# Performance work log

Hardware: AMD Instinct MI355X
Metric: run time of the kernel (lower is better)

Reference implementation:

```python
import jax, jax.numpy as jnp
import numpy as np

EMBED_DIM = 512
NUM_HEADS = 8
HEAD_DIM = EMBED_DIM // NUM_HEADS
SEQ = 1024
BSZ = 8
T1 = 0.6
T2 = 0.4
MAX_NEG = -jnp.finfo(jnp.float32).max


def setup_inputs() -> dict:
    key = jax.random.key(0)
    ks = jax.random.split(key, 10)
    shp = (SEQ, BSZ, EMBED_DIM)
    inv = 1.0 / np.sqrt(EMBED_DIM)
    return {
        "query": jax.random.normal(ks[0], shp, jnp.float32),
        "key": jax.random.normal(ks[1], shp, jnp.float32),
        "value": jax.random.normal(ks[2], shp, jnp.float32),
        "query_sem": jax.random.normal(ks[3], shp, jnp.float32),
        "key_sem": jax.random.normal(ks[4], shp, jnp.float32),
        "sem_map": jax.random.uniform(ks[5], (SEQ, SEQ), jnp.float32),
        "in_proj_weight": jax.random.normal(ks[6], (3 * EMBED_DIM, EMBED_DIM), jnp.float32) * inv,
        "in_proj_bias": jnp.zeros((3 * EMBED_DIM,), jnp.float32),
        "out_proj_weight": jax.random.normal(ks[7], (EMBED_DIM, EMBED_DIM), jnp.float32) * inv,
        "out_proj_bias": jnp.zeros((EMBED_DIM,), jnp.float32),
    }


def _heads(x):
    # [T, B, E] -> [B*H, T, head_dim]
    T, B, E = x.shape
    return jnp.transpose(x.reshape(T, B * NUM_HEADS, HEAD_DIM), (1, 0, 2))


def _attn_path(qx, kx, vx, sem_map, Wi, bi, Wo, bo, ssa):
    # packed in-projection (generic path: q, k, v are distinct tensors)
    Wq, Wk, Wv = jnp.split(Wi, 3, axis=0)
    bq, bk, bv = jnp.split(bi, 3)
    q = _heads(qx @ Wq.T + bq)
    k = _heads(kx @ Wk.T + bk)
    v = _heads(vx @ Wv.T + bv)
    scale = 1.0 / np.sqrt(HEAD_DIM)
    scores = jnp.einsum("bte,bse->bts", q * scale, k)  # [B*H, T, S]
    scores = jnp.where(sem_map[None, :, :] < 0.5, MAX_NEG, scores)
    if ssa:
        # keep only the argmax entry per row, others set to max_neg
        idx = jnp.argmax(scores, axis=-1)  # [B*H, T]
        keep = jnp.arange(scores.shape[-1])[None, None, :] == idx[..., None]
        scores = jnp.where(keep, scores, MAX_NEG)
    w = jax.nn.softmax(scores, axis=-1)
    o = jnp.einsum("bts,bse->bte", w, v)  # [B*H, T, head_dim]
    o = jnp.transpose(o, (1, 0, 2)).reshape(SEQ, BSZ, EMBED_DIM)
    return o @ Wo.T + bo


def reference(query, key, value, query_sem, key_sem, sem_map, in_proj_weight, in_proj_bias, out_proj_weight, out_proj_bias):
    # SCA: semantic q/k attend, style value
    x_sca = _attn_path(query_sem, key_sem, value, sem_map, in_proj_weight, in_proj_bias, out_proj_weight, out_proj_bias, ssa=False)
    # SSA: content/style q/k, hard-argmax sparsified attention
    x_ssa = _attn_path(query, key, value, sem_map, in_proj_weight, in_proj_bias, out_proj_weight, out_proj_bias, ssa=True)
    return T1 * x_sca + T2 * x_ssa
```

## Files before the change

kernel.cpp:

```cpp
#include <hip/hip_runtime.h>
#include <float.h>


namespace {
constexpr int kSeq = 1024;
constexpr int kBsz = 8;
constexpr int kEmb = 512;
constexpr int kHD  = 64;
constexpr float kT1 = 0.6f;
constexpr float kT2 = 0.4f;
constexpr float kScale = 0.125f;
constexpr float kMargin = 0.125f;
constexpr int kCap = 256;
}

typedef short bf16x8 __attribute__((ext_vector_type(8)));
typedef float f32x4  __attribute__((ext_vector_type(4)));

union FragU { uint4 u4; bf16x8 f; uint u[4]; };

__device__ __forceinline__ ushort f2bf(float f) {
  uint u = __float_as_uint(f);
  u += 0x7fff + ((u >> 16) & 1);
  return (ushort)(u >> 16);
}
__device__ __forceinline__ uint pack2(float lo, float hi) {
  return (uint)f2bf(lo) | ((uint)f2bf(hi) << 16);
}
__device__ __forceinline__ float bf2f(uint h) {
  return __uint_as_float(h << 16);
}
__device__ __forceinline__ uint monokey(float v) {
  uint u = __float_as_uint(v);
  return (u & 0x80000000u) ? ~u : (u | 0x80000000u);
}

__global__ void smask_prep(const float* __restrict__ SEM,
                           unsigned long long* __restrict__ SMASK) {
  const int t = blockIdx.x;
  const int w4 = threadIdx.x >> 6;
  const int lane = threadIdx.x & 63;
#pragma unroll
  for (int i = 0; i < 4; ++i) {
    const int word = (w4 << 2) + i;
    const float v = SEM[t * kSeq + (word << 6) + lane];
    unsigned long long m = __ballot(v >= 0.5f);
    if (lane == 0) SMASK[t * 16 + word] = m;
  }
}

__global__ __launch_bounds__(256, 4) void proj_v4(
    const float* __restrict__ Xq, const float* __restrict__ Xk,
    const float* __restrict__ W, const float* __restrict__ bias,
    float* __restrict__ OutQ, float* __restrict__ OutK,
    ushort* __restrict__ ShQ, ushort* __restrict__ ShK)
{
  __shared__ float As[32 * 132];
  __shared__ float Bs[32 * 68];

  const int z = blockIdx.z;
  const float* X = z ? Xk : Xq;
  float* Out = z ? OutK : OutQ;
  ushort* shadow = z ? ShK : ShQ;
  const int woff = z << 9;
  const float sscale = z ? 1.0f : kScale;

  const int mBase = blockIdx.x << 7;
  const int nBase = blockIdx.y << 6;
  const int tid = threadIdx.x;
  const int tx = tid & 15;
  const int my = tid >> 4;
  const int ar = tid >> 1, ah = (tid & 1) << 4;
  const int br = tid >> 2, bk = (tid & 3) << 3;

  float acc[8][4];
#pragma unroll
  for (int i = 0; i < 8; ++i)
#pragma unroll
    for (int j = 0; j < 4; ++j) acc[i][j] = 0.f;

  const float* xp = X + (size_t)(mBase + ar) * kEmb + ah;
  const float* wp = W + (size_t)(woff + nBase + br) * kEmb + bk;

  float4 a0 = ((const float4*)xp)[0];
  float4 a1 = ((const float4*)xp)[1];
  float4 a2 = ((const float4*)xp)[2];
  float4 a3 = ((const float4*)xp)[3];
  float4 b0 = ((const float4*)wp)[0];
  float4 b1 = ((const float4*)wp)[1];

  for (int k0 = 0; k0 < kEmb; k0 += 32) {
    __syncthreads();
    {
      float av[16] = {a0.x, a0.y, a0.z, a0.w, a1.x, a1.y, a1.z, a1.w,
                      a2.x, a2.y, a2.z, a2.w, a3.x, a3.y, a3.z, a3.w};
#pragma unroll
      for (int i = 0; i < 16; ++i) As[(ah + i) * 132 + ar] = av[i];
      float bv[8] = {b0.x, b0.y, b0.z, b0.w, b1.x, b1.y, b1.z, b1.w};
#pragma unroll
      for (int i = 0; i < 8; ++i) Bs[(bk + i) * 68 + br] = bv[i];
    }
    __syncthreads();

    const int kn = k0 + 32;
    if (kn < kEmb) {
      a0 = ((const float4*)(xp + kn))[0];
      a1 = ((const float4*)(xp + kn))[1];
      a2 = ((const float4*)(xp + kn))[2];
      a3 = ((const float4*)(xp + kn))[3];
      b0 = ((const float4*)(wp + kn))[0];
      b1 = ((const float4*)(wp + kn))[1];
    }

#pragma unroll 8
    for (int k = 0; k < 32; ++k) {
      float4 A0 = *(const float4*)&As[k * 132 + (my << 3)];
      float4 A1 = *(const float4*)&As[k * 132 + (my << 3) + 4];
      float4 Bv = *(const float4*)&Bs[k * 68 + (tx << 2)];
      float aa[8] = {A0.x, A0.y, A0.z, A0.w, A1.x, A1.y, A1.z, A1.w};
      float bb[4] = {Bv.x, Bv.y, Bv.z, Bv.w};
#pragma unroll
      for (int i = 0; i < 8; ++i)
#pragma unroll
        for (int j = 0; j < 4; ++j)
          acc[i][j] = fmaf(aa[i], bb[j], acc[i][j]);
    }
  }

#pragma unroll
  for (int i = 0; i < 8; ++i) {
    const int m = mBase + (my << 3) + i;
#pragma unroll
    for (int j = 0; j < 4; ++j) {
      const int n = nBase + (tx << 2) + j;
      const float v = acc[i][j] + bias[woff + n];
      const int oi = (((m & 7) << 3) + (n >> 6)) * (kSeq * kHD) +
                     ((m >> 3) << 6) + (n & 63);
      Out[oi] = v;
      shadow[oi] = f2bf(v * sscale);
    }
  }
}

__global__ __launch_bounds__(256, 2) void gemm_bf16(
    const float* __restrict__ X0, const float* __restrict__ X1,
    const float* __restrict__ X2, const ushort* __restrict__ X16,
    const float* __restrict__ W, const float* __restrict__ bias,
    float* __restrict__ OutF, ushort* __restrict__ Out16,
    int woffBase, int aMode, int outMode, float scale0)
{
  __shared__ uint As[128 * 20];
  __shared__ uint Bs[64 * 20];

  const int z = blockIdx.z;
  const float* X = (z == 0) ? X0 : (z == 1) ? X1 : X2;
  const int woff = woffBase + (z << 9);
  const float scale = (z == 0) ? scale0 : 1.0f;
  const size_t zoff = (size_t)z * ((size_t)kSeq * kBsz * kEmb);

  const int mBase = blockIdx.x << 7;
  const int nBase = blockIdx.y << 6;
  const int tid = threadIdx.x;
  const int w = tid >> 6;
  const int l = tid & 63;
  const int l15 = l & 15;
  const int quad = l >> 4;
  const int wm = w & 1, wn = w >> 1;

  const int srow = tid >> 1;
  const int shalf = tid & 1;

  f32x4 acc[4][2];
#pragma unroll
  for (int mi = 0; mi < 4; ++mi)
#pragma unroll
    for (int ni = 0; ni < 2; ++ni) acc[mi][ni] = (f32x4){0.f, 0.f, 0.f, 0.f};

  uint4 qa0, qa1;
  float4 ra0, ra1, ra2, ra3;
  float4 rb0, rb1, rb2, rb3;

#define GLOAD(kk) do {                                                     \
    if (aMode == 2) {                                                      \
      const uint* src_ = (const uint*)X16 + (size_t)(mBase + srow) * 256 + \
                         ((kk) >> 1) + (shalf << 3);                       \
      qa0 = ((const uint4*)src_)[0];                                       \
      qa1 = ((const uint4*)src_)[1];                                       \
    } else {                                                               \
      const float* xp_ = X + (size_t)(mBase + srow) * kEmb + (kk) +        \
                         (shalf << 4);                                     \
      ra0 = ((const float4*)xp_)[0];                                       \
      ra1 = ((const float4*)xp_)[1];                                       \
      ra2 = ((const float4*)xp_)[2];                                       \
      ra3 = ((const float4*)xp_)[3];                                       \
    }                                                                      \
    if (tid < 128) {                                                       \
      const float* wp_ = W + (size_t)(woff + nBase + srow) * kEmb + (kk) + \
                         (shalf << 4);                                     \
      rb0 = ((const float4*)wp_)[0];                                       \
      rb1 = ((const float4*)wp_)[1];                                       \
      rb2 = ((const float4*)wp_)[2];                                       \
      rb3 = ((const float4*)wp_)[3];                                       \
    }                                                                      \
  } while (0)

  GLOAD(0);

  for (int k0 = 0; k0 < kEmb; k0 += 32) {
    uint4 ah0, ah1, bw0, bw1;
    if (aMode == 2) {
      ah0 = qa0; ah1 = qa1;
    } else {
      ah0 = make_uint4(pack2(ra0.x, ra0.y), pack2(ra0.z, ra0.w),
                       pack2(ra1.x, ra1.y), pack2(ra1.z, ra1.w));
      ah1 = make_uint4(pack2(ra2.x, ra2.y), pack2(ra2.z, ra2.w),
                       pack2(ra3.x, ra3.y), pack2(ra3.z, ra3.w));
    }
    if (tid < 128) {
      bw0 = make_uint4(pack2(rb0.x, rb0.y), pack2(rb0.z, rb0.w),
                       pack2(rb1.x, rb1.y), pack2(rb1.z, rb1.w));
      bw1 = make_uint4(pack2(rb2.x, rb2.y), pack2(rb2.z, rb2.w),
                       pack2(rb3.x, rb3.y), pack2(rb3.z, rb3.w));
    }
    __syncthreads();
    {
      uint* dst = As + srow * 20 + (shalf << 3);
      ((uint4*)dst)[0] = ah0;
      ((uint4*)dst)[1] = ah1;
      if (tid < 128) {
        uint* db = Bs + srow * 20 + (shalf << 3);
        ((uint4*)db)[0] = bw0;
        ((uint4*)db)[1] = bw1;
      }
    }
    __syncthreads();

    if (k0 + 32 < kEmb) GLOAD(k0 + 32);

    FragU aF[4], bF[2];
#pragma unroll
    for (int ni = 0; ni < 2; ++ni)
      bF[ni].u4 = *(const uint4*)(Bs + ((wn << 5) + (ni << 4) + l15) * 20 + (quad << 2));
#pragma unroll
    for (int mi = 0; mi < 4; ++mi)
      aF[mi].u4 = *(const uint4*)(As + ((wm << 6) + (mi << 4) + l15) * 20 + (quad << 2));
#pragma unroll
    for (int mi = 0; mi < 4; ++mi)
#pragma unroll
      for (int ni = 0; ni < 2; ++ni)
        acc[mi][ni] = __builtin_amdgcn_mfma_f32_16x16x32_bf16(
            aF[mi].f, bF[ni].f, acc[mi][ni], 0, 0, 0);
  }
#undef GLOAD

#pragma unroll
  for (int ni = 0; ni < 2; ++ni) {
    const int n = nBase + (wn << 5) + (ni << 4) + l15;
    const float bv = bias[woff + n];
#pragma unroll
    for (int mi = 0; mi < 4; ++mi) {
#pragma unroll
      for (int r = 0; r < 4; ++r) {
        const int m = mBase + (wm << 6) + (mi << 4) + (quad << 2) + r;
        const float v = acc[mi][ni][r] + bv;
        if (outMode == 0) {
          OutF[(size_t)m * kEmb + n] = v;
        } else {
          const int oi = (((m & 7) << 3) + (n >> 6)) * (kSeq * kHD) +
                         ((m >> 3) << 6) + (n & 63);
          Out16[zoff + oi] = f2bf(v * scale);
        }
      }
    }
  }
}

__global__ __launch_bounds__(256, 4) void sca_mfma2(
    const ushort* __restrict__ Q16, const ushort* __restrict__ K16,
    const ushort* __restrict__ V16,
    const unsigned long long* __restrict__ SMASK,
    ushort* __restrict__ MIX16)
{
  __shared__ uint ks[64 * 36];
  __shared__ uint vt[64 * 36];
  __shared__ uint ps[4][16 * 36];

  const int t0  = blockIdx.x << 6;
  const int bh  = blockIdx.y;
  const int tid = threadIdx.x;
  const int w    = tid >> 6;
  const int l    = tid & 63;
  const int l15  = l & 15;
  const int quad = l >> 4;

  const uint* Qu = (const uint*)Q16 + (size_t)bh * (kSeq * 32);
  const uint* Ku = (const uint*)K16 + (size_t)bh * (kSeq * 32);
  const uint* Vu = (const uint*)V16 + (size_t)bh * (kSeq * 32);

  FragU qf0, qf1;
  {
    const uint* qrow = Qu + (size_t)(t0 + (w << 4) + l15) * 32;
    qf0.u4 = *(const uint4*)(qrow + (quad << 2));
    qf1.u4 = *(const uint4*)(qrow + 16 + (quad << 2));
  }

  f32x4 oacc[4];
#pragma unroll
  for (int nt = 0; nt < 4; ++nt) oacc[nt] = (f32x4){0.f, 0.f, 0.f, 0.f};
  float den[4] = {0.f, 0.f, 0.f, 0.f};

  uint* psw = ps[w];

  const int sl = tid >> 2, c = tid & 3;
  const int p = tid >> 3, c7 = tid & 7;

  uint4 pk0 = ((const uint4*)(Ku + (size_t)sl * 32 + (c << 3)))[0];
  uint4 pk1 = ((const uint4*)(Ku + (size_t)sl * 32 + (c << 3)))[1];
  uint4 pv0 = *(const uint4*)(Vu + (size_t)(p << 1) * 32 + (c7 << 2));
  uint4 pv1 = *(const uint4*)(Vu + (size_t)(p << 1) * 32 + (c7 << 2) + 32);

  for (int s0 = 0, tile = 0; s0 < kSeq; s0 += 64, ++tile) {
    __syncthreads();
    {
      uint* dst = ks + sl * 36 + (c << 3);
      ((uint4*)dst)[0] = pk0;
      ((uint4*)dst)[1] = pk1;
    }
    {
      FragU A, B;
      A.u4 = pv0;
      B.u4 = pv1;
      const int Wp = (p + ((c7 & 3) << 2)) & 31;
#pragma unroll
      for (int i = 0; i < 8; ++i) {
        uint ai = (A.u[i >> 1] >> ((i & 1) << 4)) & 0xFFFF;
        uint bi = (B.u[i >> 1] >> ((i & 1) << 4)) & 0xFFFF;
        vt[((c7 << 3) + i) * 36 + Wp] = ai | (bi << 16);
      }
    }
    __syncthreads();

    if (s0 + 64 < kSeq) {
      const uint* kp = Ku + (size_t)(s0 + 64 + sl) * 32 + (c << 3);
      pk0 = ((const uint4*)kp)[0];
      pk1 = ((const uint4*)kp)[1];
      const uint* va = Vu + (size_t)(s0 + 64 + (p << 1)) * 32 + (c7 << 2);
      pv0 = *(const uint4*)va;
      pv1 = *(const uint4*)(va + 32);
    }

    unsigned long long wv[4];
#pragma unroll
    for (int r = 0; r < 4; ++r)
      wv[r] = SMASK[(size_t)(t0 + (w << 4) + (quad << 2) + r) * 16 + tile];

#pragma unroll
    for (int st = 0; st < 4; ++st) {
      f32x4 sacc = (f32x4){0.f, 0.f, 0.f, 0.f};
      const int srow = (st << 4) + l15;
      FragU kf0, kf1;
      kf0.u4 = *(const uint4*)(ks + srow * 36 + (quad << 2));
      kf1.u4 = *(const uint4*)(ks + srow * 36 + 16 + (quad << 2));
      sacc = __builtin_amdgcn_mfma_f32_16x16x32_bf16(qf0.f, kf0.f, sacc, 0, 0, 0);
      sacc = __builtin_amdgcn_mfma_f32_16x16x32_bf16(qf1.f, kf1.f, sacc, 0, 0, 0);

#pragma unroll
      for (int r = 0; r < 4; ++r) {
        const int trow = (quad << 2) + r;
        const uint bit = (uint)(wv[r] >> ((st << 4) + l15)) & 1u;
        const float val = bit ? __expf(sacc[r]) : 0.f;
        den[r] += val;
        const int W  = (st << 3) + (l15 >> 1);
        const int Wp = (W + (((trow >> 3) & 1) << 3)) & 31;
        ushort* p16 = (ushort*)(psw + trow * 36 + Wp);
        p16[l15 & 1] = f2bf(val);
      }
    }
#pragma unroll
    for (int ch = 0; ch < 2; ++ch) {
      FragU pf;
      const int pw = ((ch << 4) + (quad << 2) + (((l15 >> 3) & 1) << 3)) & 31;
      pf.u4 = *(const uint4*)(psw + l15 * 36 + pw);
#pragma unroll
      for (int nt = 0; nt < 4; ++nt) {
        const int d = (nt << 4) + l15;
        const int vw = ((ch << 4) + (quad << 2) + (((d >> 3) & 3) << 2)) & 31;
        FragU vf;
        vf.u4 = *(const uint4*)(vt + d * 36 + vw);
        oacc[nt] = __builtin_amdgcn_mfma_f32_16x16x32_bf16(pf.f, vf.f, oacc[nt], 0, 0, 0);
      }
    }
  }

#pragma unroll
  for (int r = 0; r < 4; ++r) {
    float d = den[r];
    d += __shfl_xor(d, 1);
    d += __shfl_xor(d, 2);
    d += __shfl_xor(d, 4);
    d += __shfl_xor(d, 8);
    den[r] = kT1 / d;
  }
  const int b = bh >> 3, h = bh & 7;
#pragma unroll
  for (int nt = 0; nt < 4; ++nt) {
#pragma unroll
    for (int r = 0; r < 4; ++r) {
      const int t = t0 + (w << 4) + (quad << 2) + r;
      const int d = (nt << 4) + l15;
      MIX16[(size_t)(t * kBsz + b) * kEmb + (h << 6) + d] =
          f2bf(oacc[nt][r] * den[r]);
    }
  }
}

__global__ __launch_bounds__(512, 2) void ssa_v3(
    const ushort* __restrict__ Q16, const ushort* __restrict__ K16,
    const float* __restrict__ Qf, const float* __restrict__ Kf,
    const ushort* __restrict__ V16,
    const unsigned long long* __restrict__ SMASK,
    ushort* __restrict__ MIX16)
{
  __shared__ uint ks[64 * 36];
  __shared__ uint2 list[8][kCap];
  __shared__ float thrL[8][16];
  __shared__ unsigned long long key64L[8][16];
  __shared__ uint cnt[8];

  const int t0  = blockIdx.x << 7;
  const int bh  = blockIdx.y;
  const int tid = threadIdx.x;
  const int w    = tid >> 6;
  const int l    = tid & 63;
  const int l15  = l & 15;
  const int quad = l >> 4;

  if (tid < 8) cnt[tid] = 0;
  if (tid < 128) ((unsigned long long*)key64L)[tid] = 0ull;

  const uint* Qu = (const uint*)Q16 + (size_t)bh * (kSeq * 32);
  const uint* Ku = (const uint*)K16 + (size_t)bh * (kSeq * 32);

  FragU qf0, qf1;
  {
    const uint* qrow = Qu + (size_t)(t0 + (w << 4) + l15) * 32;
    qf0.u4 = *(const uint4*)(qrow + (quad << 2));
    qf1.u4 = *(const uint4*)(qrow + 16 + (quad << 2));
  }

  float m4[4] = {-FLT_MAX, -FLT_MAX, -FLT_MAX, -FLT_MAX};

  const int krow = tid >> 3, kc = tid & 7;
  uint4 pk = *(const uint4*)(Ku + (size_t)krow * 32 + (kc << 2));

  for (int s0 = 0, tile = 0; s0 < kSeq; s0 += 64, ++tile) {
    __syncthreads();
    *(uint4*)(ks + krow * 36 + (kc << 2)) = pk;
    __syncthreads();

    if (s0 + 64 < kSeq)
      pk = *(const uint4*)(Ku + (size_t)(s0 + 64 + krow) * 32 + (kc << 2));

    unsigned long long wv[4];
#pragma unroll
    for (int r = 0; r < 4; ++r)
      wv[r] = SMASK[(size_t)(t0 + (w << 4) + (quad << 2) + r) * 16 + tile];

    f32x4 sv[4];
#pragma unroll
    for (int st = 0; st < 4; ++st) {
      f32x4 sacc = (f32x4){0.f, 0.f, 0.f, 0.f};
      const int srow = (st << 4) + l15;
      FragU kf0, kf1;
      kf0.u4 = *(const uint4*)(ks + srow * 36 + (quad << 2));
      kf1.u4 = *(const uint4*)(ks + srow * 36 + 16 + (quad << 2));
      sacc = __builtin_amdgcn_mfma_f32_16x16x32_bf16(qf0.f, kf0.f, sacc, 0, 0, 0);
      sacc = __builtin_amdgcn_mfma_f32_16x16x32_bf16(qf1.f, kf1.f, sacc, 0, 0, 0);
      sv[st] = sacc;
#pragma unroll
      for (int r = 0; r < 4; ++r) {
        const uint bit = (uint)(wv[r] >> ((st << 4) + l15)) & 1u;
        if (bit) m4[r] = fmaxf(m4[r], sacc[r]);
      }
    }
#pragma unroll
    for (int r = 0; r < 4; ++r) {
      float m = m4[r];
      m = fmaxf(m, __shfl_xor(m, 1));
      m = fmaxf(m, __shfl_xor(m, 2));
      m = fmaxf(m, __shfl_xor(m, 4));
      m = fmaxf(m, __shfl_xor(m, 8));
      m4[r] = m;
    }
#pragma unroll
    for (int st = 0; st < 4; ++st) {
#pragma unroll
      for (int r = 0; r < 4; ++r) {
        const uint bit = (uint)(wv[r] >> ((st << 4) + l15)) & 1u;
        const float x = sv[st][r];
        if (bit && x >= m4[r] - kMargin) {
          uint idx = atomicAdd(&cnt[w], 1u);
          if (idx < (uint)kCap) {
            const int rowid = (quad << 2) + r;
            const int s = s0 + (st << 4) + l15;
            list[w][idx] = make_uint2(__float_as_uint(x),
                                      ((uint)rowid << 10) | (uint)s);
          }
        }
      }
    }
  }

  if (l15 == 0) {
#pragma unroll
    for (int r = 0; r < 4; ++r) thrL[w][(quad << 2) + r] = m4[r] - kMargin;
  }
  __syncthreads();

  const uint n = min(cnt[w], (uint)kCap);
  const float* Qbf = Qf + (size_t)bh * (kSeq * kHD);
  const float* Kbf = Kf + (size_t)bh * (kSeq * kHD);
  for (uint base = 0; base < n; base += 64) {
    const uint e = base + (uint)l;
    if (e < n) {
      const uint2 ent = list[w][e];
      const uint rowid = ent.y >> 10;
      const uint s = ent.y & 1023u;
      const float xv = __uint_as_float(ent.x);
      if (xv >= thrL[w][rowid]) {
        const int t = t0 + (w << 4) + (int)rowid;
        const float* qe = Qbf + (size_t)t * kHD;
        const float* ke = Kbf + (size_t)s * kHD;
        float p0 = 0.f, p1 = 0.f, p2 = 0.f, p3 = 0.f;
#pragma unroll
        for (int i = 0; i < 16; ++i) {
          float4 qq = *(const float4*)(qe + (i << 2));
          float4 kk = *(const float4*)(ke + (i << 2));
          p0 = fmaf(qq.x, kk.x, p0);
          p1 = fmaf(qq.y, kk.y, p1);
          p2 = fmaf(qq.z, kk.z, p2);
          p3 = fmaf(qq.w, kk.w, p3);
        }
        const float acc = ((p0 + p1) + (p2 + p3)) * kScale;
        const unsigned long long key =
            ((unsigned long long)monokey(acc) << 16) |
            (unsigned long long)(1023u - s);
        atomicMax(&key64L[w][rowid], key);
      }
    }
  }
  __syncthreads();

  const int b = bh >> 3, h = bh & 7;
  const uint* Vu = (const uint*)V16 + (size_t)bh * (kSeq * 32);
#pragma unroll
  for (int r = 0; r < 4; ++r) {
    const int rowid = (quad << 2) + r;
    const unsigned long long key = key64L[w][rowid];
    const uint s = 1023u - (uint)(key & 0xFFFFull);
    const uint2 vv = *(const uint2*)(Vu + (size_t)s * 32 + (l15 << 1));
    const int t = t0 + (w << 4) + rowid;
    uint* op = (uint*)MIX16 + ((size_t)(t * kBsz + b) * kEmb + (h << 6)) / 2 + (l15 << 1);
    uint2 o = *(uint2*)op;
    float o0 = bf2f(o.x & 0xFFFF) + kT2 * bf2f(vv.x & 0xFFFF);
    float o1 = bf2f(o.x >> 16)    + kT2 * bf2f(vv.x >> 16);
    float o2 = bf2f(o.y & 0xFFFF) + kT2 * bf2f(vv.y & 0xFFFF);
    float o3 = bf2f(o.y >> 16)    + kT2 * bf2f(vv.y >> 16);
    *(uint2*)op = make_uint2(pack2(o0, o1), pack2(o2, o3));
  }
}

extern "C" void kernel_launch(void* const* d_in, const int* in_sizes, int n_in,
                              void* d_out, int out_size, void* d_ws, size_t ws_size,
                              hipStream_t stream) {
  const float* query  = (const float*)d_in[0];
  const float* key    = (const float*)d_in[1];
  const float* value  = (const float*)d_in[2];
  const float* qsem   = (const float*)d_in[3];
  const float* ksem   = (const float*)d_in[4];
  const float* semmap = (const float*)d_in[5];
  const float* Wi     = (const float*)d_in[6];
  const float* bi     = (const float*)d_in[7];
  const float* Wo     = (const float*)d_in[8];
  const float* bo     = (const float*)d_in[9];
  float* out = (float*)d_out;

  char* ws = (char*)d_ws;
  unsigned long long* SMASK = (unsigned long long*)ws;          ws += 1024 * 16 * 8;
  ushort* Q16  = (ushort*)ws;  ws += (size_t)64 * kSeq * kHD * 2;
  ushort* K16  = (ushort*)ws;  ws += (size_t)64 * kSeq * kHD * 2;
  ushort* V16  = (ushort*)ws;  ws += (size_t)64 * kSeq * kHD * 2;
  ushort* MIX16 = (ushort*)ws; ws += (size_t)kSeq * kBsz * kEmb * 2;
  float* P1 = (float*)ws;      ws += (size_t)64 * kSeq * kHD * 4;
  float* P0 = out;

  const dim3 gp(64, 8, 2);
  const dim3 g3(64, 8, 3);
  const dim3 gb(64, 8);
  const dim3 gs(16, 64);
  const dim3 gv(8, 64);

  smask_prep<<<1024, 256, 0, stream>>>(semmap, SMASK);
  gemm_bf16<<<g3, 256, 0, stream>>>(qsem, ksem, value, nullptr, Wi, bi,
                                    nullptr, Q16, 0, 0, 1, kScale);
  sca_mfma2<<<gs, 256, 0, stream>>>(Q16, K16, V16, SMASK, MIX16);
  proj_v4<<<gp, 256, 0, stream>>>(query, key, Wi, bi, P0, P1, Q16, K16);
  ssa_v3<<<gv, 512, 0, stream>>>(Q16, K16, P0, P1, V16, SMASK, MIX16);
  gemm_bf16<<<gb, 256, 0, stream>>>(nullptr, nullptr, nullptr, MIX16, Wo, bo,
                                    out, nullptr, 0, 2, 0, 1.0f);
}
```

Measured before the change: 412.6 us.

## Rewrite fp32 projection to stream weights via scalar loads into SGPRs

Replaces the LDS-tiled fp32 projection GEMM with a version that stages only the activation tile in shared memory. Weights are wave-uniform and are fetched with inline s_load_dwordx16 into scalar registers. Each lane accumulates one row across 32 output columns. This removes the B-tile LDS traffic and the transposed shared stores. In exchange, each column waits on a blocking scalar-load wait, which may expose memory latency.

```diff
diff --git a/kernel.cpp b/kernel.cpp
--- a/kernel.cpp
+++ b/kernel.cpp
@@ -16,6 +16,7 @@
 
 typedef short bf16x8 __attribute__((ext_vector_type(8)));
 typedef float f32x4  __attribute__((ext_vector_type(4)));
+typedef float f32x16 __attribute__((ext_vector_type(16)));
 
 union FragU { uint4 u4; bf16x8 f; uint u[4]; };
 
@@ -49,14 +50,13 @@
   }
 }
 
-__global__ __launch_bounds__(256, 4) void proj_v4(
+__global__ __launch_bounds__(256, 4) void proj_v7(
     const float* __restrict__ Xq, const float* __restrict__ Xk,
     const float* __restrict__ W, const float* __restrict__ bias,
     float* __restrict__ OutQ, float* __restrict__ OutK,
     ushort* __restrict__ ShQ, ushort* __restrict__ ShK)
 {
-  __shared__ float As[32 * 132];
-  __shared__ float Bs[32 * 68];
+  __shared__ float As[128 * 36];
 
   const int z = blockIdx.z;
   const float* X = z ? Xk : Xq;
@@ -68,77 +68,84 @@
   const int mBase = blockIdx.x << 7;
   const int nBase = blockIdx.y << 6;
   const int tid = threadIdx.x;
-  const int tx = tid & 15;
-  const int my = tid >> 4;
-  const int ar = tid >> 1, ah = (tid & 1) << 4;
-  const int br = tid >> 2, bk = (tid & 3) << 3;
-
-  float acc[8][4];
-#pragma unroll
-  for (int i = 0; i < 8; ++i)
-#pragma unroll
-    for (int j = 0; j < 4; ++j) acc[i][j] = 0.f;
-
-  const float* xp = X + (size_t)(mBase + ar) * kEmb + ah;
-  const float* wp = W + (size_t)(woff + nBase + br) * kEmb + bk;
-
-  float4 a0 = ((const float4*)xp)[0];
-  float4 a1 = ((const float4*)xp)[1];
-  float4 a2 = ((const float4*)xp)[2];
-  float4 a3 = ((const float4*)xp)[3];
-  float4 b0 = ((const float4*)wp)[0];
-  float4 b1 = ((const float4*)wp)[1];
+  const int l   = tid & 63;
+  const int wu  = __builtin_amdgcn_readfirstlane(tid >> 6);
+  const int rg  = wu & 1;
+  const int cg  = wu >> 1;
+  const int row = (rg << 6) + l;
+
+  const int sr = tid >> 1;
+  const int sh = (tid & 1) << 4;
+
+  const float* xp = X + (size_t)(mBase + sr) * kEmb + sh;
+  const float* wbase = W + (size_t)(woff + nBase + (cg << 5)) * kEmb;
+
+  float acc[32];
+#pragma unroll
+  for (int c = 0; c < 32; ++c) acc[c] = 0.f;
+
+  float4 st0 = ((const float4*)xp)[0];
+  float4 st1 = ((const float4*)xp)[1];
+  float4 st2 = ((const float4*)xp)[2];
+  float4 st3 = ((const float4*)xp)[3];
 
   for (int k0 = 0; k0 < kEmb; k0 += 32) {
     __syncthreads();
     {
-      float av[16] = {a0.x, a0.y, a0.z, a0.w, a1.x, a1.y, a1.z, a1.w,
-                      a2.x, a2.y, a2.z, a2.w, a3.x, a3.y, a3.z, a3.w};
-#pragma unroll
-      for (int i = 0; i < 16; ++i) As[(ah + i) * 132 + ar] = av[i];
-      float bv[8] = {b0.x, b0.y, b0.z, b0.w, b1.x, b1.y, b1.z, b1.w};
-#pragma unroll
-      for (int i = 0; i < 8; ++i) Bs[(bk + i) * 68 + br] = bv[i];
+      float* dst = &As[sr * 36 + sh];
+      *(float4*)(dst + 0)  = st0;
+      *(float4*)(dst + 4)  = st1;
+      *(float4*)(dst + 8)  = st2;
+      *(float4*)(dst + 12) = st3;
     }
     __syncthreads();
 
     const int kn = k0 + 32;
     if (kn < kEmb) {
-      a0 = ((const float4*)(xp + kn))[0];
-      a1 = ((const float4*)(xp + kn))[1];
-      a2 = ((const float4*)(xp + kn))[2];
-      a3 = ((const float4*)(xp + kn))[3];
-      b0 = ((const float4*)(wp + kn))[0];
-      b1 = ((const float4*)(wp + kn))[1];
-    }
-
-#pragma unroll 8
-    for (int k = 0; k < 32; ++k) {
-      float4 A0 = *(const float4*)&As[k * 132 + (my << 3)];
-      float4 A1 = *(const float4*)&As[k * 132 + (my << 3) + 4];
-      float4 Bv = *(const float4*)&Bs[k * 68 + (tx << 2)];
-      float aa[8] = {A0.x, A0.y, A0.z, A0.w, A1.x, A1.y, A1.z, A1.w};
-      float bb[4] = {Bv.x, Bv.y, Bv.z, Bv.w};
-#pragma unroll
-      for (int i = 0; i < 8; ++i)
-#pragma unroll
-        for (int j = 0; j < 4; ++j)
-          acc[i][j] = fmaf(aa[i], bb[j], acc[i][j]);
-    }
-  }
-
-#pragma unroll
-  for (int i = 0; i < 8; ++i) {
-    const int m = mBase + (my << 3) + i;
-#pragma unroll
-    for (int j = 0; j < 4; ++j) {
-      const int n = nBase + (tx << 2) + j;
-      const float v = acc[i][j] + bias[woff + n];
-      const int oi = (((m & 7) << 3) + (n >> 6)) * (kSeq * kHD) +
-                     ((m >> 3) << 6) + (n & 63);
-      Out[oi] = v;
-      shadow[oi] = f2bf(v * sscale);
-    }
+      st0 = ((const float4*)(xp + kn))[0];
+      st1 = ((const float4*)(xp + kn))[1];
+      st2 = ((const float4*)(xp + kn))[2];
+      st3 = ((const float4*)(xp + kn))[3];
+    }
+
+    float af[32];
+#pragma unroll
+    for (int j = 0; j < 8; ++j) {
+      float4 t = *(const float4*)&As[row * 36 + (j << 2)];
+      af[(j << 2) + 0] = t.x;
+      af[(j << 2) + 1] = t.y;
+      af[(j << 2) + 2] = t.z;
+      af[(j << 2) + 3] = t.w;
+    }
+
+#pragma unroll
+    for (int c = 0; c < 32; ++c) {
+      const float* wcol = wbase + (size_t)c * kEmb + k0;
+      f32x16 b0, b1;
+      asm volatile(
+          "s_load_dwordx16 %0, %2, 0x0\n\t"
+          "s_load_dwordx16 %1, %2, 0x40\n\t"
+          "s_waitcnt lgkmcnt(0)"
+          : "=s"(b0), "=s"(b1)
+          : "s"(wcol));
+#pragma unroll
+      for (int kk = 0; kk < 16; ++kk)
+        acc[c] = fmaf(af[kk], b0[kk], acc[c]);
+#pragma unroll
+      for (int kk = 0; kk < 16; ++kk)
+        acc[c] = fmaf(af[16 + kk], b1[kk], acc[c]);
+    }
+  }
+
+  const int m = mBase + row;
+#pragma unroll
+  for (int c = 0; c < 32; ++c) {
+    const int n = nBase + (cg << 5) + c;
+    const float v = acc[c] + bias[woff + n];
+    const int oi = (((m & 7) << 3) + (n >> 6)) * (kSeq * kHD) +
+                   ((m >> 3) << 6) + (n & 63);
+    Out[oi] = v;
+    shadow[oi] = f2bf(v * sscale);
   }
 }
 
@@ -604,7 +611,7 @@
   gemm_bf16<<<g3, 256, 0, stream>>>(qsem, ksem, value, nullptr, Wi, bi,
                                     nullptr, Q16, 0, 0, 1, kScale);
   sca_mfma2<<<gs, 256, 0, stream>>>(Q16, K16, V16, SMASK, MIX16);
-  proj_v4<<<gp, 256, 0, stream>>>(query, key, Wi, bi, P0, P1, Q16, K16);
+  proj_v7<<<gp, 256, 0, stream>>>(query, key, Wi, bi, P0, P1, Q16, K16);
   ssa_v3<<<gv, 512, 0, stream>>>(Q16, K16, P0, P1, V16, SMASK, MIX16);
   gemm_bf16<<<gb, 256, 0, stream>>>(nullptr, nullptr, nullptr, MIX16, Wo, bo,
                                     out, nullptr, 0, 2, 0, 1.0f);
```

New measurement: 559.5 us. +35.6%, slower.
